# Kernel optimization log

Measured on AMD Instinct MI355X. Metric: run time of the kernel, lower is better.

## Reference

```python
import jax, jax.numpy as jnp
import numpy as np

BN_EPS = 1e-5


def _gin_layer(x, src, dst, W1, b1, W2, b2, gamma, beta):
    N = x.shape[0]
    # scatter-add neighbor aggregation (GINConv with eps=0)
    agg = jax.ops.segment_sum(x[src], dst, num_segments=N)
    h = x + agg
    # MLP: Linear -> ReLU -> Linear
    h = jax.nn.relu(h @ W1 + b1) @ W2 + b2
    # BatchNorm1d (training-mode batch statistics, biased variance)
    mean = jnp.mean(h, axis=0)
    var = jnp.mean(jnp.square(h - mean), axis=0)
    h = (h - mean) * jax.lax.rsqrt(var + BN_EPS) * gamma + beta
    return jax.nn.relu(h)


def setup_inputs() -> dict:
    key = jax.random.key(0)
    ks = jax.random.split(key, 16)
    N, E, F_IN, H, L, G, T = 100000, 400000, 128, 256, 5, 4096, 12
    x = jax.random.normal(ks[0], (N, F_IN), dtype=jnp.float32)
    edge_index = jax.random.randint(ks[1], (2, E), 0, N, dtype=jnp.int64)
    batch_idx = jnp.sort(jax.random.randint(ks[2], (N,), 0, G, dtype=jnp.int64))
    s = 0.02
    inp = {
        "x": x,
        "edge_index": edge_index,
        "batch_idx": batch_idx,
        "num_graphs": G,
        # layer 0: 128 -> 256
        "W1_0": jax.random.normal(ks[3], (F_IN, H), dtype=jnp.float32) * s,
        "b1_0": jnp.zeros((H,), jnp.float32),
        "W2_0": jax.random.normal(ks[4], (H, H), dtype=jnp.float32) * s,
        "b2_0": jnp.zeros((H,), jnp.float32),
        "gamma_0": jnp.ones((H,), jnp.float32),
        "beta_0": jnp.zeros((H,), jnp.float32),
        # layers 1..4 stacked: 256 -> 256
        "W1s": jax.random.normal(ks[5], (L - 1, H, H), dtype=jnp.float32) * s,
        "b1s": jnp.zeros((L - 1, H), jnp.float32),
        "W2s": jax.random.normal(ks[6], (L - 1, H, H), dtype=jnp.float32) * s,
        "b2s": jnp.zeros((L - 1, H), jnp.float32),
        "gammas": jnp.ones((L - 1, H), jnp.float32),
        "betas": jnp.zeros((L - 1, H), jnp.float32),
        # predictor
        "Wp1": jax.random.normal(ks[7], (H, H), dtype=jnp.float32) * s,
        "bp1": jnp.zeros((H,), jnp.float32),
        "Wp2": jax.random.normal(ks[8], (H, T), dtype=jnp.float32) * s,
        "bp2": jnp.zeros((T,), jnp.float32),
    }
    return inp


def reference(x, edge_index, batch_idx, num_graphs,
              W1_0, b1_0, W2_0, b2_0, gamma_0, beta_0,
              W1s, b1s, W2s, b2s, gammas, betas,
              Wp1, bp1, Wp2, bp2):
    src, dst = edge_index[0], edge_index[1]
    h = _gin_layer(x, src, dst, W1_0, b1_0, W2_0, b2_0, gamma_0, beta_0)
    for i in range(W1s.shape[0]):
        h = _gin_layer(h, src, dst, W1s[i], b1s[i], W2s[i], b2s[i], gammas[i], betas[i])
    # global mean pool over graphs
    sums = jax.ops.segment_sum(h, batch_idx, num_segments=num_graphs)
    counts = jax.ops.segment_sum(jnp.ones((h.shape[0],), h.dtype), batch_idx, num_segments=num_graphs)
    g = sums / jnp.maximum(counts, 1.0)[:, None]
    # predictor MLP (dropout=0 in eval)
    out = jax.nn.relu(g @ Wp1 + bp1) @ Wp2 + bp2
    return out
```

## Files before the change

kernel.cpp:

```cpp
#include <hip/hip_runtime.h>


typedef __attribute__((ext_vector_type(4))) float f32x4;
typedef __attribute__((ext_vector_type(8))) _Float16 f16x8;

__device__ __forceinline__ float h2f(unsigned short u) {
  _Float16 h; __builtin_memcpy(&h, &u, 2); return (float)h;
}
__device__ __forceinline__ unsigned short f2h16(float f) {
  _Float16 h = (_Float16)f; unsigned short u; __builtin_memcpy(&u, &h, 2); return u;
}
__device__ __forceinline__ unsigned short f2b(float f) {
  union { float f; unsigned int i; } c; c.f = f;
  unsigned int x = c.i;
  return (unsigned short)((x + 0x7fffu + ((x >> 16) & 1u)) >> 16);
}
__device__ __forceinline__ float lin(const void* p, long long i, int wf32) {
  if (wf32) return ((const float*)p)[i];
  union { unsigned int i; float f; } c;
  c.i = ((unsigned int)((const unsigned short*)p)[i]) << 16;
  return c.f;
}
__device__ __forceinline__ int ldidx(const int* p, long long i, int w64) {
  return w64 ? p[2 * i] : p[i];
}

__device__ __forceinline__ void gload_lds16(const void* g, void* l) {
  __builtin_amdgcn_global_load_lds(
      (const __attribute__((address_space(1))) unsigned int*)g,
      (__attribute__((address_space(3))) unsigned int*)l, 16, 0, 0);
}

__global__ void detect_k(const int* __restrict__ edge, const unsigned short* __restrict__ xa,
                         int* __restrict__ flags) {
  if (threadIdx.x != 0 || blockIdx.x != 0) return;
  int nzOdd = 0;
  for (int t = 0; t < 256; t++) if (edge[2 * t + 1] != 0) nzOdd++;
  flags[0] = (nzOdd == 0) ? 1 : 0;
  int plaus = 0;
  for (int t = 0; t < 64; t++) {
    unsigned short w = xa[2 * t];
    int e = (w >> 7) & 0xFF;
    if (w == 0 || (e >= 0x70 && e <= 0x85)) plaus++;
  }
  flags[1] = (plaus < 32) ? 1 : 0;
}

__global__ void zero_i32_k(int* __restrict__ p, int n) {
  int i = blockIdx.x * blockDim.x + threadIdx.x;
  if (i < n) p[i] = 0;
}

__global__ void prep_k(const void* __restrict__ b1, const void* __restrict__ b2,
                       const void* __restrict__ gm, const void* __restrict__ bt, int eoff,
                       float* __restrict__ pb1, float* __restrict__ pb2,
                       float* __restrict__ pg, float* __restrict__ pb,
                       float* __restrict__ gsum, const int* __restrict__ flags) {
  int wf32 = flags[1], t = threadIdx.x;
  pb1[t] = lin(b1, (long long)eoff + t, wf32);
  pb2[t] = lin(b2, (long long)eoff + t, wf32);
  pg[t]  = lin(gm, (long long)eoff + t, wf32);
  pb[t]  = lin(bt, (long long)eoff + t, wf32);
  gsum[t] = 0.f; gsum[256 + t] = 0.f;
}
__global__ void copy256_k(const void* __restrict__ src, int eoff, float* __restrict__ dst,
                          const int* __restrict__ flags) {
  dst[threadIdx.x] = lin(src, (long long)eoff + threadIdx.x, flags[1]);
}

__global__ void transpose_off_k(const void* __restrict__ src, long long eoff,
                                unsigned short* __restrict__ dst, int R, int C,
                                const int* __restrict__ flags) {
  int wf32 = flags[1];
  __shared__ unsigned short t[32][33];
  int bx = blockIdx.x * 32, by = blockIdx.y * 32;
  int x = bx + threadIdx.x;
  for (int i = 0; i < 32; i += 8) {
    int y = by + threadIdx.y + i;
    if (y < R && x < C)
      t[threadIdx.y + i][threadIdx.x] = f2h16(lin(src, eoff + (long long)y * C + x, wf32));
  }
  __syncthreads();
  int x2 = by + threadIdx.x;
  for (int i = 0; i < 32; i += 8) {
    int y = bx + threadIdx.y + i;
    if (y < C && x2 < R) dst[(long long)y * R + x2] = t[threadIdx.x][threadIdx.y + i];
  }
}

__global__ void hist_k(const int* __restrict__ edge, int E, int* __restrict__ cnt,
                       const int* __restrict__ flags) {
  int w64 = flags[0];
  int e = blockIdx.x * blockDim.x + threadIdx.x;
  if (e < E) atomicAdd(&cnt[ldidx(edge, (long long)E + e, w64)], 1);
}
#define SCAN_CHUNK 1024
__global__ void scan1_k(const int* __restrict__ in, int* __restrict__ out,
                        int* __restrict__ partials, int n) {
  __shared__ int sh[256];
  int tid = threadIdx.x;
  int base = blockIdx.x * SCAN_CHUNK + tid * 4;
  int v[4]; int tsum = 0;
#pragma unroll
  for (int i = 0; i < 4; i++) { v[i] = (base + i < n) ? in[base + i] : 0; tsum += v[i]; }
  sh[tid] = tsum; __syncthreads();
  for (int off = 1; off < 256; off <<= 1) {
    int t = (tid >= off) ? sh[tid - off] : 0;
    __syncthreads();
    sh[tid] += t;
    __syncthreads();
  }
  int run = sh[tid] - tsum;
#pragma unroll
  for (int i = 0; i < 4; i++) { if (base + i < n) out[base + i] = run; run += v[i]; }
  if (tid == 255) partials[blockIdx.x] = sh[255];
}
__global__ void scan2_k(int* partials, int B) {
  __shared__ int sh[256];
  int tid = threadIdx.x;
  int orig = (tid < B) ? partials[tid] : 0;
  sh[tid] = orig; __syncthreads();
  for (int off = 1; off < 256; off <<= 1) {
    int t = (tid >= off) ? sh[tid - off] : 0;
    __syncthreads();
    sh[tid] += t;
    __syncthreads();
  }
  if (tid < B) partials[tid] = sh[tid] - orig;
}
__global__ void scan3_k(int* __restrict__ out, const int* __restrict__ partials,
                        int n, int total) {
  int base = blockIdx.x * SCAN_CHUNK + threadIdx.x * 4;
  int add = partials[blockIdx.x];
#pragma unroll
  for (int i = 0; i < 4; i++) { if (base + i < n) out[base + i] += add; }
  if (blockIdx.x == 0 && threadIdx.x == 0) out[n] = total;
}
__global__ void fill_k(const int* __restrict__ edge, int E, const int* __restrict__ rowptr,
                       int* __restrict__ cnt, int* __restrict__ colidx,
                       const int* __restrict__ flags) {
  int w64 = flags[0];
  int e = blockIdx.x * blockDim.x + threadIdx.x;
  if (e >= E) return;
  int s = ldidx(edge, e, w64);
  int d = ldidx(edge, (long long)E + e, w64);
  int p = atomicAdd(&cnt[d], 1);
  colidx[rowptr[d] + p] = s;
}
__global__ void graph_bounds_k(const int* __restrict__ b, int Nn, int G,
                               int* __restrict__ gstart, const int* __restrict__ flags) {
  int w64 = flags[0];
  int g = blockIdx.x * blockDim.x + threadIdx.x;
  if (g > G) return;
  int lo = 0, hi = Nn;
  while (lo < hi) {
    int mid = (lo + hi) >> 1;
    if (ldidx(b, mid, w64) < g) lo = mid + 1; else hi = mid;
  }
  gstart[g] = lo;
}

__global__ void convert_k(const void* __restrict__ x, unsigned short* __restrict__ xh,
                          long long n, const int* __restrict__ flags) {
  int wf32 = flags[1];
  long long base = ((long long)blockIdx.x * blockDim.x + threadIdx.x) * 4;
  if (base >= n) return;
#pragma unroll
  for (int k = 0; k < 4; k++) xh[base + k] = f2h16(lin(x, base + k, wf32));
}

template <int LPN, int APPLY>
__global__ void gather_fused_k(const unsigned short* __restrict__ src,
                               const float* __restrict__ scale, const float* __restrict__ shift,
                               const int* __restrict__ rowptr, const int* __restrict__ colidx,
                               unsigned short* __restrict__ u, int Nn) {
  const int F = LPN * 8;
  int gid = blockIdx.x * blockDim.x + threadIdx.x;
  int node = gid / LPN;
  if (node >= Nn) return;
  int fb = (gid % LPN) * 8;
  float sc[8], sh[8];
  if (APPLY) {
#pragma unroll
    for (int k = 0; k < 8; k++) { sc[k] = scale[fb + k]; sh[k] = shift[fb + k]; }
  }
  float acc[8];
  {
    uint4 raw = *(const uint4*)(src + (long long)node * F + fb);
    unsigned int ws[4] = {raw.x, raw.y, raw.z, raw.w};
#pragma unroll
    for (int k = 0; k < 8; k++) {
      float xv = h2f((unsigned short)((ws[k >> 1] >> ((k & 1) * 16)) & 0xffff));
      acc[k] = APPLY ? fmaxf(xv * sc[k] + sh[k], 0.f) : xv;
    }
  }
  int s = rowptr[node], e = rowptr[node + 1];
  for (int j = s; j < e; j++) {
    long long nb = colidx[j];
    uint4 raw = *(const uint4*)(src + nb * F + fb);
    unsigned int ws[4] = {raw.x, raw.y, raw.z, raw.w};
#pragma unroll
    for (int k = 0; k < 8; k++) {
      float xv = h2f((unsigned short)((ws[k >> 1] >> ((k & 1) * 16)) & 0xffff));
      acc[k] += APPLY ? fmaxf(xv * sc[k] + sh[k], 0.f) : xv;
    }
  }
  uint4 o;
  unsigned int wo[4];
#pragma unroll
  for (int p = 0; p < 4; p++)
    wo[p] = (unsigned int)f2h16(acc[2 * p]) | ((unsigned int)f2h16(acc[2 * p + 1]) << 16);
  o.x = wo[0]; o.y = wo[1]; o.z = wo[2]; o.w = wo[3];
  *(uint4*)(u + (long long)node * F + fb) = o;
}

template <int KIN>
__device__ __forceinline__ void stage_tile_lds(
    const unsigned short* __restrict__ A, long long row0, int M,
    unsigned char* R, int tid) {
  const int lane = tid & 63, wave = tid >> 6;
  constexpr int ROWB = 2 * KIN;
  constexpr int CHUNKS = ROWB / 16;
  constexpr int NISSUE = (128 * ROWB) / (8 * 1024);
#pragma unroll
  for (int j = 0; j < NISSUE; j++) {
    int slot = j * 8 + wave;
    int baseRow = (slot * 1024) / ROWB;
    int row = baseRow + lane / CHUNKS;
    int ci = lane % CHUNKS;
    int c = ci ^ (row & 7);
    long long rg = row0 + row;
    if (rg >= M) rg = M - 1;
    gload_lds16(A + rg * KIN + c * 8, R + slot * 1024);
  }
}

template <int KIN>
__global__ __launch_bounds__(512, 4) void fused_layer_k(
    const unsigned short* __restrict__ A, const unsigned short* __restrict__ W1t,
    const unsigned short* __restrict__ W2t, const float* __restrict__ b1,
    const float* __restrict__ b2, unsigned short* __restrict__ V,
    int M, float* __restrict__ gsum) {
  __shared__ __align__(16) unsigned char R[65536];
  const int tid = threadIdx.x;
  const int lane = tid & 63, wave = tid >> 6;
  const int l15 = lane & 15, lq = lane >> 4;
  const int wn = wave >> 1, wm = wave & 1;
  const int nb0 = wn * 64, mb0 = wm * 64;
  constexpr int KT1 = KIN / 32;
  const long long m0 = (long long)blockIdx.x * 128;

  stage_tile_lds<KIN>(A, m0, M, R, tid);
  __syncthreads();

  f32x4 acc[4][4] = {};
#pragma unroll 1
  for (int kt = 0; kt < KT1; kt++) {
    f16x8 wf[4], uf[4];
#pragma unroll
    for (int r = 0; r < 4; r++)
      wf[r] = *(const f16x8*)(W1t + (long long)(nb0 + 16 * r + l15) * KIN + kt * 32 + lq * 8);
#pragma unroll
    for (int c = 0; c < 4; c++) {
      int m = mb0 + 16 * c + l15;
      uf[c] = *(const f16x8*)(R + m * (2 * KIN) + 16 * ((kt * 4 + lq) ^ (m & 7)));
    }
#pragma unroll
    for (int r = 0; r < 4; r++)
#pragma unroll
      for (int c = 0; c < 4; c++)
        acc[r][c] = __builtin_amdgcn_mfma_f32_16x16x32_f16(wf[r], uf[c], acc[r][c], 0, 0, 0);
  }
  __syncthreads();
#pragma unroll
  for (int r = 0; r < 4; r++) {
    int nbase = nb0 + 16 * r + lq * 4;
    float4 bv = *(const float4*)(b1 + nbase);
#pragma unroll
    for (int c = 0; c < 4; c++) {
      int m = mb0 + 16 * c + l15;
      unsigned int h0 = f2h16(fmaxf(acc[r][c][0] + bv.x, 0.f));
      unsigned int h1v = f2h16(fmaxf(acc[r][c][1] + bv.y, 0.f));
      unsigned int h2v = f2h16(fmaxf(acc[r][c][2] + bv.z, 0.f));
      unsigned int h3 = f2h16(fmaxf(acc[r][c][3] + bv.w, 0.f));
      uint2 pk; pk.x = h0 | (h1v << 16); pk.y = h2v | (h3 << 16);
      int by = m * 512 + 16 * ((nbase >> 3) ^ (m & 7)) + ((nbase & 7) << 1);
      *(uint2*)(R + by) = pk;
    }
  }
  __syncthreads();
  f32x4 acc2[4][4] = {};
#pragma unroll 1
  for (int kt = 0; kt < 8; kt++) {
    f16x8 wf[4], hf[4];
#pragma unroll
    for (int r = 0; r < 4; r++)
      wf[r] = *(const f16x8*)(W2t + (long long)(nb0 + 16 * r + l15) * 256 + kt * 32 + lq * 8);
#pragma unroll
    for (int c = 0; c < 4; c++) {
      int m = mb0 + 16 * c + l15;
      hf[c] = *(const f16x8*)(R + m * 512 + 16 * ((kt * 4 + lq) ^ (m & 7)));
    }
#pragma unroll
    for (int r = 0; r < 4; r++)
#pragma unroll
      for (int c = 0; c < 4; c++)
        acc2[r][c] = __builtin_amdgcn_mfma_f32_16x16x32_f16(wf[r], hf[c], acc2[r][c], 0, 0, 0);
  }
  __syncthreads();
#pragma unroll
  for (int r = 0; r < 4; r++) {
    int nbase = nb0 + 16 * r + lq * 4;
    float4 bv = *(const float4*)(b2 + nbase);
#pragma unroll
    for (int c = 0; c < 4; c++) {
      int m = mb0 + 16 * c + l15;
      unsigned int h0 = f2h16(acc2[r][c][0] + bv.x);
      unsigned int h1v = f2h16(acc2[r][c][1] + bv.y);
      unsigned int h2v = f2h16(acc2[r][c][2] + bv.z);
      unsigned int h3 = f2h16(acc2[r][c][3] + bv.w);
      uint2 pk; pk.x = h0 | (h1v << 16); pk.y = h2v | (h3 << 16);
      int by = m * 512 + 16 * ((nbase >> 3) ^ (m & 7)) + ((nbase & 7) << 1);
      *(uint2*)(R + by) = pk;
    }
  }
  __syncthreads();
  const int c32 = tid & 31, rg = tid >> 5;
  float s8[8] = {}, q8[8] = {};
#pragma unroll
  for (int k = 0; k < 8; k++) {
    int m = rg * 8 + k;
    uint4 vw = *(const uint4*)(R + m * 512 + 16 * (c32 ^ (m & 7)));
    long long grow = m0 + m;
    if (grow < M) {
      *(uint4*)(V + grow * 256 + c32 * 8) = vw;
      unsigned int ws[4] = {vw.x, vw.y, vw.z, vw.w};
#pragma unroll
      for (int kk = 0; kk < 8; kk++) {
        float xv = h2f((unsigned short)((ws[kk >> 1] >> ((kk & 1) * 16)) & 0xffff));
        s8[kk] += xv; q8[kk] += xv * xv;
      }
    }
  }
  __syncthreads();
  float* shf = (float*)R;
#pragma unroll
  for (int kk = 0; kk < 8; kk++) {
    int col = c32 * 8 + kk;
    shf[col * 17 + rg] = s8[kk];
    shf[4352 + col * 17 + rg] = q8[kk];
  }
  __syncthreads();
  if (tid < 256) {
    float tot = 0.f;
#pragma unroll
    for (int g = 0; g < 16; g++) tot += shf[tid * 17 + g];
    atomicAdd(&gsum[tid], tot);
  } else {
    int col = tid - 256; float tot = 0.f;
#pragma unroll
    for (int g = 0; g < 16; g++) tot += shf[4352 + col * 17 + g];
    atomicAdd(&gsum[256 + col], tot);
  }
}

#define SA 40
#define SP 136
__global__ __launch_bounds__(256) void gemm_k(
    const unsigned short* __restrict__ A, const unsigned short* __restrict__ Bt,
    const float* __restrict__ bias, unsigned short* __restrict__ C,
    int M, int K, int relu, float* __restrict__ gsum) {
  __shared__ __align__(16) unsigned short smem[128 * SP];
  unsigned short* As = smem;
  unsigned short* Bs = smem + 128 * SA;
  int m0 = blockIdx.x * 128, n0 = blockIdx.y * 128;
  int tid = threadIdx.x;
  int wave = tid >> 6, lane = tid & 63;
  int wm = (wave >> 1) * 64, wnn = (wave & 1) * 64;
  int lrow = lane & 15, lqq = lane >> 4;
  f32x4 acc[4][4] = {};
  int ktiles = K >> 5;
  int srow = tid >> 2;
  int ch8 = (tid & 3) << 3;
  int rowA0 = m0 + srow;      rowA0 = rowA0 < M ? rowA0 : M - 1;
  int rowA1 = m0 + srow + 64; rowA1 = rowA1 < M ? rowA1 : M - 1;
  const unsigned short* pa0 = A + (long long)rowA0 * K + ch8;
  const unsigned short* pa1 = A + (long long)rowA1 * K + ch8;
  const unsigned short* pq0 = Bt + (long long)(n0 + srow) * K + ch8;
  const unsigned short* pq1 = Bt + (long long)(n0 + srow + 64) * K + ch8;
  uint4 va0 = *(const uint4*)pa0, va1 = *(const uint4*)pa1;
  uint4 vb0 = *(const uint4*)pq0, vb1 = *(const uint4*)pq1;
  int lo0 = srow * SA + ch8, lo1 = (srow + 64) * SA + ch8;
  for (int kt = 0; kt < ktiles; ++kt) {
    __syncthreads();
    *(uint4*)(As + lo0) = va0;
    *(uint4*)(As + lo1) = va1;
    *(uint4*)(Bs + lo0) = vb0;
    *(uint4*)(Bs + lo1) = vb1;
    __syncthreads();
    f16x8 af[4], bf[4];
#pragma unroll
    for (int r = 0; r < 4; r++)
      af[r] = *(const f16x8*)(As + (wm + 16 * r + lrow) * SA + lqq * 8);
#pragma unroll
    for (int c = 0; c < 4; c++)
      bf[c] = *(const f16x8*)(Bs + (wnn + 16 * c + lrow) * SA + lqq * 8);
    if (kt + 1 < ktiles) {
      int kb = (kt + 1) << 5;
      va0 = *(const uint4*)(pa0 + kb); va1 = *(const uint4*)(pa1 + kb);
      vb0 = *(const uint4*)(pq0 + kb); vb1 = *(const uint4*)(pq1 + kb);
    }
#pragma unroll
    for (int r = 0; r < 4; r++)
#pragma unroll
      for (int c = 0; c < 4; c++)
        acc[r][c] = __builtin_amdgcn_mfma_f32_16x16x32_f16(af[r], bf[c], acc[r][c], 0, 0, 0);
  }
  __syncthreads();
  unsigned short* Ct = smem;
#pragma unroll
  for (int c = 0; c < 4; c++) {
    int col = wnn + 16 * c + lrow;
    float bv = bias[n0 + col];
#pragma unroll
    for (int r = 0; r < 4; r++) {
      int rbase = wm + 16 * r + lqq * 4;
#pragma unroll
      for (int i = 0; i < 4; i++) {
        float v = acc[r][c][i] + bv;
        if (relu) v = fmaxf(v, 0.f);
        Ct[(rbase + i) * SP + col] = f2h16(v);
      }
    }
  }
  __syncthreads();
  int c16 = tid & 15, g = tid >> 4;
  float s8[8] = {}, q8[8] = {};
  bool dostats = (gsum != nullptr);
#pragma unroll
  for (int i = 0; i < 8; i++) {
    int row = g + i * 16;
    int grow = m0 + row;
    uint4 vw = *(const uint4*)(Ct + row * SP + c16 * 8);
    if (grow < M) {
      *(uint4*)(C + (long long)grow * 256 + n0 + c16 * 8) = vw;
      if (dostats) {
        unsigned int ws[4] = {vw.x, vw.y, vw.z, vw.w};
#pragma unroll
        for (int k = 0; k < 8; k++) {
          float xv = h2f((unsigned short)((ws[k >> 1] >> ((k & 1) * 16)) & 0xffff));
          s8[k] += xv; q8[k] += xv * xv;
        }
      }
    }
  }
  if (dostats) {
    float* shf = (float*)smem;
    __syncthreads();
#pragma unroll
    for (int k = 0; k < 8; k++) shf[(c16 * 8 + k) * 17 + g] = s8[k];
    __syncthreads();
    if (tid < 128) {
      float t = 0.f;
#pragma unroll
      for (int gg = 0; gg < 16; gg++) t += shf[tid * 17 + gg];
      atomicAdd(&gsum[n0 + tid], t);
    }
    __syncthreads();
#pragma unroll
    for (int k = 0; k < 8; k++) shf[(c16 * 8 + k) * 17 + g] = q8[k];
    __syncthreads();
    if (tid < 128) {
      float t = 0.f;
#pragma unroll
      for (int gg = 0; gg < 16; gg++) t += shf[tid * 17 + gg];
      atomicAdd(&gsum[256 + n0 + tid], t);
    }
  }
}

__global__ void bn_finalize_k(const float* __restrict__ gsum,
                              const float* __restrict__ pg, const float* __restrict__ pb,
                              int Nn, float* __restrict__ scale, float* __restrict__ shift) {
  int f = threadIdx.x;
  float inv = 1.f / (float)Nn;
  float mean = gsum[f] * inv;
  float var = fmaxf(gsum[256 + f] * inv - mean * mean, 0.f);
  float sc = pg[f] * rsqrtf(var + 1e-5f);
  scale[f] = sc;
  shift[f] = pb[f] - mean * sc;
}

__global__ void pool_fused_k(const unsigned short* __restrict__ v, const float* __restrict__ scale,
                             const float* __restrict__ shift, const int* __restrict__ gstart,
                             unsigned short* __restrict__ gout) {
  int g = blockIdx.x, f = threadIdx.x;
  int s = gstart[g], e = gstart[g + 1];
  float sc = scale[f], sh = shift[f];
  float acc = 0.f;
  for (int r = s; r < e; r++) acc += fmaxf(h2f(v[(long long)r * 256 + f]) * sc + sh, 0.f);
  gout[(long long)g * 256 + f] = f2h16(acc / fmaxf((float)(e - s), 1.f));
}
__global__ void pred2_k(const unsigned short* __restrict__ p1, const void* __restrict__ Wp2,
                        const void* __restrict__ bp2, void* __restrict__ out, int G,
                        const int* __restrict__ flags) {
  int wf32 = flags[1];
  int idx = blockIdx.x * blockDim.x + threadIdx.x;
  if (idx >= G * 12) return;
  int g = idx / 12, t = idx - g * 12;
  float acc = lin(bp2, t, wf32);
  const unsigned short* row = p1 + (long long)g * 256;
  for (int k = 0; k < 256; k++) acc += h2f(row[k]) * lin(Wp2, k * 12 + t, wf32);
  if (wf32) ((float*)out)[idx] = acc;
  else      ((unsigned short*)out)[idx] = f2b(acc);
}

extern "C" void kernel_launch(void* const* d_in, const int* in_sizes, int n_in,
                              void* d_out, int out_size, void* d_ws, size_t ws_size,
                              hipStream_t stream) {
  int wb = -1;
  for (int i = 3; i + 15 < n_in; i++) {
    if (in_sizes[i] == 32768 && in_sizes[i + 1] == 256 && in_sizes[i + 2] == 65536 &&
        in_sizes[i + 3] == 256 && in_sizes[i + 4] == 256 && in_sizes[i + 5] == 256 &&
        in_sizes[i + 6] == 262144) { wb = i; break; }
  }
  if (wb < 0) wb = (n_in >= 20) ? 4 : 3;

  const void* x      = d_in[0];
  const int*  edge   = (const int*)d_in[1];
  const int*  batch  = (const int*)d_in[2];
  const void* W1_0   = d_in[wb + 0];
  const void* b1_0   = d_in[wb + 1];
  const void* W2_0   = d_in[wb + 2];
  const void* b2_0   = d_in[wb + 3];
  const void* gamma0 = d_in[wb + 4];
  const void* beta0  = d_in[wb + 5];
  const void* W1s    = d_in[wb + 6];
  const void* b1s    = d_in[wb + 7];
  const void* W2s    = d_in[wb + 8];
  const void* b2s    = d_in[wb + 9];
  const void* gammas = d_in[wb + 10];
  const void* betas  = d_in[wb + 11];
  const void* Wp1    = d_in[wb + 12];
  const void* bp1    = d_in[wb + 13];
  const void* Wp2    = d_in[wb + 14];
  const void* bp2    = d_in[wb + 15];

  const int N = in_sizes[0] / 128;
  const int E = in_sizes[1] / 2;
  const int G = out_size / 12;
  const int H = 256;

  char* w = (char*)d_ws;
  size_t off = 0;
  auto alloc = [&](size_t bytes) -> char* {
    char* p = w + off;
    off += (bytes + 255) & ~(size_t)255;
    return p;
  };
  unsigned short* bufX  = (unsigned short*)alloc((size_t)N * H * 2);
  unsigned short* bufY  = (unsigned short*)alloc((size_t)N * H * 2);
  unsigned short* w1_0t = (unsigned short*)alloc((size_t)128 * 256 * 2);
  unsigned short* w2_0t = (unsigned short*)alloc((size_t)256 * 256 * 2);
  unsigned short* w1st  = (unsigned short*)alloc((size_t)4 * 256 * 256 * 2);
  unsigned short* w2st  = (unsigned short*)alloc((size_t)4 * 256 * 256 * 2);
  unsigned short* wp1t  = (unsigned short*)alloc((size_t)256 * 256 * 2);
  int*   rowptr   = (int*)alloc((size_t)(N + 1) * 4);
  int*   cnt      = (int*)alloc((size_t)N * 4);
  int*   colidx   = (int*)alloc((size_t)E * 4);
  int*   partials = (int*)alloc(1024 * 4);
  float* gsum     = (float*)alloc(512 * 4);
  float* bnscale  = (float*)alloc(256 * 4);
  float* bnshift  = (float*)alloc(256 * 4);
  float* pg       = (float*)alloc(256 * 4);
  float* pb       = (float*)alloc(256 * 4);
  float* pb1      = (float*)alloc(256 * 4);
  float* pb2      = (float*)alloc(256 * 4);
  int*   gstart   = (int*)alloc((size_t)(G + 1) * 4);
  int*   flags    = (int*)alloc(256);
  unsigned short* gpool = (unsigned short*)alloc((size_t)G * H * 2);
  unsigned short* p1    = (unsigned short*)alloc((size_t)G * H * 2);
  (void)ws_size; (void)n_in;

  detect_k<<<1, 64, 0, stream>>>(edge, (const unsigned short*)x, flags);

  convert_k<<<(int)(((long long)N * 128 / 4 + 255) / 256), 256, 0, stream>>>(
      x, bufY, (long long)N * 128, flags);

  dim3 tb(32, 8);
  auto transpose = [&](const void* src, long long eoff, unsigned short* dst, int R, int C) {
    transpose_off_k<<<dim3((C + 31) / 32, (R + 31) / 32), tb, 0, stream>>>(src, eoff, dst, R, C, flags);
  };
  transpose(W1_0, 0, w1_0t, 128, 256);
  transpose(W2_0, 0, w2_0t, 256, 256);
  for (int i = 0; i < 4; i++) {
    transpose(W1s, (long long)i * 65536, w1st + i * 65536, 256, 256);
    transpose(W2s, (long long)i * 65536, w2st + i * 65536, 256, 256);
  }
  transpose(Wp1, 0, wp1t, 256, 256);

  zero_i32_k<<<(N + 255) / 256, 256, 0, stream>>>(cnt, N);
  hist_k<<<(E + 255) / 256, 256, 0, stream>>>(edge, E, cnt, flags);
  int NB = (N + SCAN_CHUNK - 1) / SCAN_CHUNK;
  scan1_k<<<NB, 256, 0, stream>>>(cnt, rowptr, partials, N);
  scan2_k<<<1, 256, 0, stream>>>(partials, NB);
  scan3_k<<<NB, 256, 0, stream>>>(rowptr, partials, N, E);
  zero_i32_k<<<(N + 255) / 256, 256, 0, stream>>>(cnt, N);
  fill_k<<<(E + 255) / 256, 256, 0, stream>>>(edge, E, rowptr, cnt, colidx, flags);
  graph_bounds_k<<<(G + 1 + 255) / 256, 256, 0, stream>>>(batch, N, G, gstart, flags);

  const int ntiles = (N + 127) / 128;
  auto fused = [&](const unsigned short* Au, const unsigned short* w1, const unsigned short* w2,
                   unsigned short* Vv, int K) {
    if (K == 128)
      fused_layer_k<128><<<ntiles, 512, 0, stream>>>(Au, w1, w2, pb1, pb2, Vv, N, gsum);
    else
      fused_layer_k<256><<<ntiles, 512, 0, stream>>>(Au, w1, w2, pb1, pb2, Vv, N, gsum);
  };

  prep_k<<<1, 256, 0, stream>>>(b1_0, b2_0, gamma0, beta0, 0, pb1, pb2, pg, pb, gsum, flags);
  gather_fused_k<16, 0><<<(N * 16 + 255) / 256, 256, 0, stream>>>(
      bufY, bnscale, bnshift, rowptr, colidx, bufX, N);
  fused(bufX, w1_0t, w2_0t, bufY, 128);
  bn_finalize_k<<<1, 256, 0, stream>>>(gsum, pg, pb, N, bnscale, bnshift);
  unsigned short* cur = bufY;
  unsigned short* oth = bufX;
  for (int i = 0; i < 4; i++) {
    prep_k<<<1, 256, 0, stream>>>(b1s, b2s, gammas, betas, i * 256, pb1, pb2, pg, pb, gsum, flags);
    gather_fused_k<32, 1><<<(N * 32 + 255) / 256, 256, 0, stream>>>(
        cur, bnscale, bnshift, rowptr, colidx, oth, N);
    fused(oth, w1st + i * 65536, w2st + i * 65536, cur, 256);
    bn_finalize_k<<<1, 256, 0, stream>>>(gsum, pg, pb, N, bnscale, bnshift);
  }

  copy256_k<<<1, 256, 0, stream>>>(bp1, 0, pb1, flags);
  pool_fused_k<<<G, 256, 0, stream>>>(cur, bnscale, bnshift, gstart, gpool);
  gemm_k<<<dim3((G + 127) / 128, 2), 256, 0, stream>>>(gpool, wp1t, pb1, p1, G, 256, 1, nullptr);
  pred2_k<<<(G * 12 + 255) / 256, 256, 0, stream>>>(p1, Wp2, bp2, d_out, G, flags);
}
```

Measured before the change: 940.5 us.

## Halve fused layer row tile to 64 and shard BN stat atomics

The fused MLP kernel now processes 64 rows per block instead of 128, with each of 8 waves owning a 32-column slice. This shrinks LDS from 64KB to 36KB and accumulator registers so more blocks can be resident per CU (launch bounds 6). BatchNorm sum/sumsq atomics are spread over 32 sharded buffers reduced in bn_finalize to cut atomic contention, and s_setprio is raised around MFMA loops. Weight fragments are now reloaded from global memory twice as often per row processed, and the epilogue and staging overhead is amortized over fewer rows.

```diff
diff --git a/kernel.cpp b/kernel.cpp
--- a/kernel.cpp
+++ b/kernel.cpp
@@ -61,7 +61,7 @@
   pb2[t] = lin(b2, (long long)eoff + t, wf32);
   pg[t]  = lin(gm, (long long)eoff + t, wf32);
   pb[t]  = lin(bt, (long long)eoff + t, wf32);
-  gsum[t] = 0.f; gsum[256 + t] = 0.f;
+  for (int i = t; i < 32 * 512; i += 256) gsum[i] = 0.f;
 }
 __global__ void copy256_k(const void* __restrict__ src, int eoff, float* __restrict__ dst,
                           const int* __restrict__ flags) {
@@ -215,13 +215,13 @@
 }
 
 template <int KIN>
-__device__ __forceinline__ void stage_tile_lds(
+__device__ __forceinline__ void stage_tile64(
     const unsigned short* __restrict__ A, long long row0, int M,
     unsigned char* R, int tid) {
   const int lane = tid & 63, wave = tid >> 6;
   constexpr int ROWB = 2 * KIN;
   constexpr int CHUNKS = ROWB / 16;
-  constexpr int NISSUE = (128 * ROWB) / (8 * 1024);
+  constexpr int NISSUE = (64 * ROWB) / (8 * 1024);
 #pragma unroll
   for (int j = 0; j < NISSUE; j++) {
     int slot = j * 8 + wave;
@@ -236,49 +236,50 @@
 }
 
 template <int KIN>
-__global__ __launch_bounds__(512, 4) void fused_layer_k(
+__global__ __launch_bounds__(512, 6) void fused_layer_k(
     const unsigned short* __restrict__ A, const unsigned short* __restrict__ W1t,
     const unsigned short* __restrict__ W2t, const float* __restrict__ b1,
     const float* __restrict__ b2, unsigned short* __restrict__ V,
     int M, float* __restrict__ gsum) {
-  __shared__ __align__(16) unsigned char R[65536];
+  __shared__ __align__(16) unsigned char R[36864];
   const int tid = threadIdx.x;
   const int lane = tid & 63, wave = tid >> 6;
   const int l15 = lane & 15, lq = lane >> 4;
-  const int wn = wave >> 1, wm = wave & 1;
-  const int nb0 = wn * 64, mb0 = wm * 64;
+  const int nb0 = wave * 32;
   constexpr int KT1 = KIN / 32;
-  const long long m0 = (long long)blockIdx.x * 128;
-
-  stage_tile_lds<KIN>(A, m0, M, R, tid);
-  __syncthreads();
-
-  f32x4 acc[4][4] = {};
+  const long long m0 = (long long)blockIdx.x * 64;
+
+  stage_tile64<KIN>(A, m0, M, R, tid);
+  __syncthreads();
+
+  f32x4 acc[2][4] = {};
+  __builtin_amdgcn_s_setprio(1);
 #pragma unroll 1
   for (int kt = 0; kt < KT1; kt++) {
-    f16x8 wf[4], uf[4];
-#pragma unroll
-    for (int r = 0; r < 4; r++)
+    f16x8 wf[2], uf[4];
+#pragma unroll
+    for (int r = 0; r < 2; r++)
       wf[r] = *(const f16x8*)(W1t + (long long)(nb0 + 16 * r + l15) * KIN + kt * 32 + lq * 8);
 #pragma unroll
     for (int c = 0; c < 4; c++) {
-      int m = mb0 + 16 * c + l15;
+      int m = 16 * c + l15;
       uf[c] = *(const f16x8*)(R + m * (2 * KIN) + 16 * ((kt * 4 + lq) ^ (m & 7)));
     }
 #pragma unroll
-    for (int r = 0; r < 4; r++)
+    for (int r = 0; r < 2; r++)
 #pragma unroll
       for (int c = 0; c < 4; c++)
         acc[r][c] = __builtin_amdgcn_mfma_f32_16x16x32_f16(wf[r], uf[c], acc[r][c], 0, 0, 0);
   }
-  __syncthreads();
-#pragma unroll
-  for (int r = 0; r < 4; r++) {
+  __builtin_amdgcn_s_setprio(0);
+  __syncthreads();
+#pragma unroll
+  for (int r = 0; r < 2; r++) {
     int nbase = nb0 + 16 * r + lq * 4;
     float4 bv = *(const float4*)(b1 + nbase);
 #pragma unroll
     for (int c = 0; c < 4; c++) {
-      int m = mb0 + 16 * c + l15;
+      int m = 16 * c + l15;
       unsigned int h0 = f2h16(fmaxf(acc[r][c][0] + bv.x, 0.f));
       unsigned int h1v = f2h16(fmaxf(acc[r][c][1] + bv.y, 0.f));
       unsigned int h2v = f2h16(fmaxf(acc[r][c][2] + bv.z, 0.f));
@@ -289,32 +290,34 @@
     }
   }
   __syncthreads();
-  f32x4 acc2[4][4] = {};
+  f32x4 acc2[2][4] = {};
+  __builtin_amdgcn_s_setprio(1);
 #pragma unroll 1
   for (int kt = 0; kt < 8; kt++) {
-    f16x8 wf[4], hf[4];
-#pragma unroll
-    for (int r = 0; r < 4; r++)
+    f16x8 wf[2], hf[4];
+#pragma unroll
+    for (int r = 0; r < 2; r++)
       wf[r] = *(const f16x8*)(W2t + (long long)(nb0 + 16 * r + l15) * 256 + kt * 32 + lq * 8);
 #pragma unroll
     for (int c = 0; c < 4; c++) {
-      int m = mb0 + 16 * c + l15;
+      int m = 16 * c + l15;
       hf[c] = *(const f16x8*)(R + m * 512 + 16 * ((kt * 4 + lq) ^ (m & 7)));
     }
 #pragma unroll
-    for (int r = 0; r < 4; r++)
+    for (int r = 0; r < 2; r++)
 #pragma unroll
       for (int c = 0; c < 4; c++)
         acc2[r][c] = __builtin_amdgcn_mfma_f32_16x16x32_f16(wf[r], hf[c], acc2[r][c], 0, 0, 0);
   }
-  __syncthreads();
-#pragma unroll
-  for (int r = 0; r < 4; r++) {
+  __builtin_amdgcn_s_setprio(0);
+  __syncthreads();
+#pragma unroll
+  for (int r = 0; r < 2; r++) {
     int nbase = nb0 + 16 * r + lq * 4;
     float4 bv = *(const float4*)(b2 + nbase);
 #pragma unroll
     for (int c = 0; c < 4; c++) {
-      int m = mb0 + 16 * c + l15;
+      int m = 16 * c + l15;
       unsigned int h0 = f2h16(acc2[r][c][0] + bv.x);
       unsigned int h1v = f2h16(acc2[r][c][1] + bv.y);
       unsigned int h2v = f2h16(acc2[r][c][2] + bv.z);
@@ -328,8 +331,8 @@
   const int c32 = tid & 31, rg = tid >> 5;
   float s8[8] = {}, q8[8] = {};
 #pragma unroll
-  for (int k = 0; k < 8; k++) {
-    int m = rg * 8 + k;
+  for (int k = 0; k < 4; k++) {
+    int m = rg * 4 + k;
     uint4 vw = *(const uint4*)(R + m * 512 + 16 * (c32 ^ (m & 7)));
     long long grow = m0 + m;
     if (grow < M) {
@@ -351,16 +354,17 @@
     shf[4352 + col * 17 + rg] = q8[kk];
   }
   __syncthreads();
+  float* gb = gsum + (blockIdx.x & 31) * 512;
   if (tid < 256) {
     float tot = 0.f;
 #pragma unroll
     for (int g = 0; g < 16; g++) tot += shf[tid * 17 + g];
-    atomicAdd(&gsum[tid], tot);
+    atomicAdd(&gb[tid], tot);
   } else {
     int col = tid - 256; float tot = 0.f;
 #pragma unroll
     for (int g = 0; g < 16; g++) tot += shf[4352 + col * 17 + g];
-    atomicAdd(&gsum[256 + col], tot);
+    atomicAdd(&gb[256 + col], tot);
   }
 }
 
@@ -483,9 +487,12 @@
                               const float* __restrict__ pg, const float* __restrict__ pb,
                               int Nn, float* __restrict__ scale, float* __restrict__ shift) {
   int f = threadIdx.x;
+  float s = 0.f, q = 0.f;
+#pragma unroll 4
+  for (int b = 0; b < 32; b++) { s += gsum[b * 512 + f]; q += gsum[b * 512 + 256 + f]; }
   float inv = 1.f / (float)Nn;
-  float mean = gsum[f] * inv;
-  float var = fmaxf(gsum[256 + f] * inv - mean * mean, 0.f);
+  float mean = s * inv;
+  float var = fmaxf(q * inv - mean * mean, 0.f);
   float sc = pg[f] * rsqrtf(var + 1e-5f);
   scale[f] = sc;
   shift[f] = pb[f] - mean * sc;
@@ -569,7 +576,7 @@
   int*   cnt      = (int*)alloc((size_t)N * 4);
   int*   colidx   = (int*)alloc((size_t)E * 4);
   int*   partials = (int*)alloc(1024 * 4);
-  float* gsum     = (float*)alloc(512 * 4);
+  float* gsum     = (float*)alloc(32 * 512 * 4);
   float* bnscale  = (float*)alloc(256 * 4);
   float* bnshift  = (float*)alloc(256 * 4);
   float* pg       = (float*)alloc(256 * 4);
@@ -609,7 +616,7 @@
   fill_k<<<(E + 255) / 256, 256, 0, stream>>>(edge, E, rowptr, cnt, colidx, flags);
   graph_bounds_k<<<(G + 1 + 255) / 256, 256, 0, stream>>>(batch, N, G, gstart, flags);
 
-  const int ntiles = (N + 127) / 128;
+  const int ntiles = (N + 63) / 64;
   auto fused = [&](const unsigned short* Au, const unsigned short* w1, const unsigned short* w2,
                    unsigned short* Vv, int K) {
     if (K == 128)
```

After: 897.2 us. 1.05x faster.
